# Kernel optimization log

Hardware: AMD Instinct MI355X
Metric: run time of the kernel (lower is better)

The kernel has to match this reference:

```python
import jax, jax.numpy as jnp
import numpy as np

B, S, D, H = 8, 4096, 1024, 16
DH = D // H  # head size = 64


def setup_inputs() -> dict:
    key = jax.random.key(0)
    ks = jax.random.split(key, 9)
    scale = 1.0 / np.sqrt(D)
    x = jax.random.normal(ks[0], (B, S, D), dtype=jnp.float32)
    wq = jax.random.normal(ks[1], (D, D), dtype=jnp.float32) * scale
    bq = jnp.zeros((D,), dtype=jnp.float32)
    wk = jax.random.normal(ks[2], (D, D), dtype=jnp.float32) * scale
    bk = jnp.zeros((D,), dtype=jnp.float32)
    wv = jax.random.normal(ks[3], (D, D), dtype=jnp.float32) * scale
    bv = jnp.zeros((D,), dtype=jnp.float32)
    wo = jax.random.normal(ks[4], (D, D), dtype=jnp.float32) * scale
    bo = jnp.zeros((D,), dtype=jnp.float32)
    return {"x": x, "wq": wq, "bq": bq, "wk": wk, "bk": bk,
            "wv": wv, "bv": bv, "wo": wo, "bo": bo}


def reference(x, wq, bq, wk, bk, wv, bv, wo, bo):
    b, s, d = x.shape
    # torch Linear: y = x @ W^T + b
    q = (x @ wq.T + bq).reshape(b, s, H, DH)
    k = (x @ wk.T + bk).reshape(b, s, H, DH)
    v = (x @ wv.T + bv).reshape(b, s, H, DH)
    # NOTE: original transpose_for_scores only reshapes (no permute), so
    # matmul(q, k.transpose(-1,-2)) contracts over head_size and the softmax
    # runs over the HEAD axis per token: scores shape [B, S, H, H].
    scores = jnp.einsum('bshd,bsgd->bshg', q, k) / jnp.sqrt(jnp.float32(DH))
    probs = jax.nn.softmax(scores, axis=-1)
    ctx = jnp.einsum('bshg,bsgd->bshd', probs, v).reshape(b, s, d)
    return ctx @ wo.T + bo
```

## Files before the change

### kernel.cpp

```cpp
#include <hip/hip_runtime.h>
#include <hip/hip_bf16.h>


#define DEV static __device__ __forceinline__

typedef __attribute__((ext_vector_type(8))) _Float16 fp16x8;
typedef __attribute__((ext_vector_type(4))) float f32x4;

DEV unsigned short f2h(float f) {
    union { _Float16 h; unsigned short u; } c;
    c.h = (_Float16)f;
    return c.u;
}
DEV float h2f(unsigned short u) {
    union { _Float16 h; unsigned short u; } c;
    c.u = u;
    return (float)c.h;
}

DEV void gl_lds16(const void* g, void* l) {
    __builtin_amdgcn_global_load_lds(
        (const __attribute__((address_space(1))) unsigned int*)g,
        (__attribute__((address_space(3))) unsigned int*)l, 16, 0, 0);
}

__global__ __launch_bounds__(256) void k_convert(
    const float* __restrict__ x,
    const float* __restrict__ wq, const float* __restrict__ wk,
    const float* __restrict__ wv, const float* __restrict__ wo,
    const float* __restrict__ bq, const float* __restrict__ bk,
    const float* __restrict__ bv,
    unsigned short* __restrict__ Xb, unsigned short* __restrict__ Wb,
    unsigned short* __restrict__ Wob, float* __restrict__ biasc)
{
    const int NX = 33554432 / 4;
    const int NW = 3145728 / 4;
    const int NO = 1048576 / 4;
    const int NB = 3072 / 4;
    const int total = NX + NW + NO + NB;
    for (int c = blockIdx.x * blockDim.x + threadIdx.x; c < total;
         c += gridDim.x * blockDim.x) {
        if (c < NX) {
            float4 v = ((const float4*)x)[c];
            uint2 u;
            u.x = f2h(v.x) | ((unsigned int)f2h(v.y) << 16);
            u.y = f2h(v.z) | ((unsigned int)f2h(v.w) << 16);
            ((uint2*)Xb)[c] = u;
        } else if (c < NX + NW) {
            int e = c - NX;
            const float* w = (e < 262144) ? wq : (e < 524288) ? wk : wv;
            int off = e & 262143;
            float4 v = ((const float4*)w)[off];
            uint2 u;
            u.x = f2h(v.x) | ((unsigned int)f2h(v.y) << 16);
            u.y = f2h(v.z) | ((unsigned int)f2h(v.w) << 16);
            ((uint2*)Wb)[e] = u;
        } else if (c < NX + NW + NO) {
            int e = c - NX - NW;
            float4 v = ((const float4*)wo)[e];
            uint2 u;
            u.x = f2h(v.x) | ((unsigned int)f2h(v.y) << 16);
            u.y = f2h(v.z) | ((unsigned int)f2h(v.w) << 16);
            ((uint2*)Wob)[e] = u;
        } else {
            int e = c - NX - NW - NO;
            const float* b = (e < 256) ? bq : (e < 512) ? bk : bv;
            int off = e & 255;
            ((float4*)biasc)[e] = ((const float4*)b)[off];
        }
    }
}

template <int LDA, bool OUT_F16>
__global__ __launch_bounds__(256) void k_gemm_bt(
    const unsigned short* __restrict__ A,
    const unsigned short* __restrict__ B,
    const float* __restrict__ bias,
    unsigned short* __restrict__ Ch,
    float* __restrict__ Cf,
    int ldc)
{
    __shared__ __align__(16) unsigned short As[128 * 32];
    __shared__ __align__(16) unsigned short Bs[128 * 32];

    const int tid  = threadIdx.x;
    const int lane = tid & 63;
    const int w    = tid >> 6;
    const int wr   = w >> 1, wc = w & 1;
    const int quad = lane >> 4;
    const int lr   = lane & 15;

    const int m0 = blockIdx.y * 128;
    const int n0 = blockIdx.x * 128;

    f32x4 acc[4][4];
#pragma unroll
    for (int i = 0; i < 4; ++i)
#pragma unroll
        for (int j = 0; j < 4; ++j) {
            f32x4 z = {0.f, 0.f, 0.f, 0.f};
            acc[i][j] = z;
        }

    const int id0 = tid, id1 = tid + 256;
    const int ar0 = id0 >> 2, ac0 = (id0 & 3) * 8;
    const int ar1 = id1 >> 2, ac1 = (id1 & 3) * 8;
    const unsigned short* Arow0 = A + (size_t)(m0 + ar0) * LDA + ac0;
    const unsigned short* Arow1 = A + (size_t)(m0 + ar1) * LDA + ac1;
    const unsigned short* Brow0 = B + (size_t)(n0 + ar0) * 1024 + ac0;
    const unsigned short* Brow1 = B + (size_t)(n0 + ar1) * 1024 + ac1;

    for (int k0 = 0; k0 < 1024; k0 += 32) {
        __syncthreads();
        gl_lds16(Arow0 + k0, (char*)As + id0 * 16);
        gl_lds16(Arow1 + k0, (char*)As + id1 * 16);
        gl_lds16(Brow0 + k0, (char*)Bs + id0 * 16);
        gl_lds16(Brow1 + k0, (char*)Bs + id1 * 16);
        asm volatile("s_waitcnt vmcnt(0)" ::: "memory");
        __syncthreads();

        fp16x8 a[4], b[4];
#pragma unroll
        for (int i = 0; i < 4; ++i)
            a[i] = *(const fp16x8*)(const void*)&As[(wr * 64 + i * 16 + lr) * 32 + quad * 8];
#pragma unroll
        for (int j = 0; j < 4; ++j)
            b[j] = *(const fp16x8*)(const void*)&Bs[(wc * 64 + j * 16 + lr) * 32 + quad * 8];
#pragma unroll
        for (int i = 0; i < 4; ++i)
#pragma unroll
            for (int j = 0; j < 4; ++j)
                acc[i][j] = __builtin_amdgcn_mfma_f32_16x16x32_f16(a[i], b[j], acc[i][j], 0, 0, 0);
    }

    float bj[4];
#pragma unroll
    for (int j = 0; j < 4; ++j) bj[j] = bias[n0 + wc * 64 + j * 16 + lr];
#pragma unroll
    for (int i = 0; i < 4; ++i) {
        const int mrow = m0 + wr * 64 + i * 16 + quad * 4;
#pragma unroll
        for (int j = 0; j < 4; ++j) {
            const int ncol = n0 + wc * 64 + j * 16 + lr;
#pragma unroll
            for (int r = 0; r < 4; ++r) {
                float v = acc[i][j][r] + bj[j];
                if (OUT_F16)
                    Ch[(size_t)(mrow + r) * ldc + ncol] = f2h(v);
                else
                    Cf[(size_t)(mrow + r) * ldc + ncol] = v;
            }
        }
    }
}

__global__ __launch_bounds__(256) void k_attn(unsigned short* __restrict__ qkv)
{
    __shared__ __align__(16) float sq[4][3072];
    __shared__ __align__(16) float sp[4][16 * 17];

    const int tid = threadIdx.x;
    const int wv  = tid >> 6;
    const int l   = tid & 63;
    const int t   = blockIdx.x * 4 + wv;
    unsigned short* tok = qkv + (size_t)t * 3072;

#pragma unroll
    for (int i = 0; i < 6; ++i) {
        const int e = i * 512 + l * 8;
        uint4 u = *(const uint4*)(tok + e);
        unsigned int uu[4] = {u.x, u.y, u.z, u.w};
#pragma unroll
        for (int c = 0; c < 4; ++c) {
            sq[wv][e + 2 * c]     = h2f((unsigned short)(uu[c] & 0xffff));
            sq[wv][e + 2 * c + 1] = h2f((unsigned short)(uu[c] >> 16));
        }
    }
    __syncthreads();

    const int h  = l >> 2;
    const int gq = (l & 3) * 4;
    const float4* q4 = (const float4*)&sq[wv][h * 64];
    const float4* k4 = (const float4*)&sq[wv][1024];

    float s[4] = {0.f, 0.f, 0.f, 0.f};
#pragma unroll
    for (int d4 = 0; d4 < 16; ++d4) {
        float4 qv = q4[d4];
#pragma unroll
        for (int g = 0; g < 4; ++g) {
            float4 kv = k4[(gq + g) * 16 + d4];
            s[g] += qv.x * kv.x + qv.y * kv.y + qv.z * kv.z + qv.w * kv.w;
        }
    }
#pragma unroll
    for (int g = 0; g < 4; ++g) s[g] *= 0.125f;

    float m = fmaxf(fmaxf(s[0], s[1]), fmaxf(s[2], s[3]));
    m = fmaxf(m, __shfl_xor(m, 1, 64));
    m = fmaxf(m, __shfl_xor(m, 2, 64));
    float e4[4], sum = 0.f;
#pragma unroll
    for (int g = 0; g < 4; ++g) { e4[g] = __expf(s[g] - m); sum += e4[g]; }
    sum += __shfl_xor(sum, 1, 64);
    sum += __shfl_xor(sum, 2, 64);
    const float inv = 1.0f / sum;
#pragma unroll
    for (int g = 0; g < 4; ++g) sp[wv][h * 17 + gq + g] = e4[g] * inv;
    __syncthreads();

    const int db = l & 3;
    const float4* v4 = (const float4*)&sq[wv][2048];
    float acc[16];
#pragma unroll
    for (int j = 0; j < 16; ++j) acc[j] = 0.f;
#pragma unroll
    for (int g = 0; g < 16; ++g) {
        const float p = sp[wv][h * 17 + g];
        const float4* vr = v4 + g * 16 + db * 4;
#pragma unroll
        for (int c = 0; c < 4; ++c) {
            float4 vvv = vr[c];
            acc[c * 4 + 0] += p * vvv.x;
            acc[c * 4 + 1] += p * vvv.y;
            acc[c * 4 + 2] += p * vvv.z;
            acc[c * 4 + 3] += p * vvv.w;
        }
    }

    unsigned short* dst = tok + h * 64 + db * 16;
    unsigned int o[8];
#pragma unroll
    for (int j = 0; j < 8; ++j)
        o[j] = f2h(acc[2 * j]) | ((unsigned int)f2h(acc[2 * j + 1]) << 16);
    uint4 o0 = {o[0], o[1], o[2], o[3]};
    uint4 o1 = {o[4], o[5], o[6], o[7]};
    ((uint4*)dst)[0] = o0;
    ((uint4*)dst)[1] = o1;
}

extern "C" void kernel_launch(void* const* d_in, const int* in_sizes, int n_in,
                              void* d_out, int out_size, void* d_ws, size_t ws_size,
                              hipStream_t stream)
{
    (void)in_sizes; (void)n_in; (void)out_size;

    const float* x  = (const float*)d_in[0];
    const float* wq = (const float*)d_in[1];
    const float* bq = (const float*)d_in[2];
    const float* wk = (const float*)d_in[3];
    const float* bk = (const float*)d_in[4];
    const float* wv = (const float*)d_in[5];
    const float* bv = (const float*)d_in[6];
    const float* wo = (const float*)d_in[7];
    const float* bo = (const float*)d_in[8];

    if (ws_size < 276836352ull) return;

    char* ws = (char*)d_ws;
    unsigned short* QKV  = (unsigned short*)(ws);
    unsigned short* Xb   = (unsigned short*)(ws + 201326592);
    unsigned short* Wb   = (unsigned short*)(ws + 268435456);
    unsigned short* Wob  = (unsigned short*)(ws + 274726912);
    float*          bqkv = (float*)(ws + 276824064);

    k_convert<<<2048, 256, 0, stream>>>(x, wq, wk, wv, wo, bq, bk, bv,
                                        Xb, Wb, Wob, bqkv);
    k_gemm_bt<1024, true><<<dim3(24, 256), 256, 0, stream>>>(
        Xb, Wb, bqkv, QKV, nullptr, 3072);
    k_attn<<<8192, 256, 0, stream>>>(QKV);
    k_gemm_bt<3072, false><<<dim3(8, 256), 256, 0, stream>>>(
        QKV, Wob, bo, nullptr, (float*)d_out, 1024);
}
```

Baseline: 696.7 us.

## Compute per-token head attention with fp16 MFMA instead of scalar fp32 LDS math

Rewrites the per-token head-axis attention kernel to stage Q and K as fp16 in padded LDS rows and compute the 16x16 score matrix with a 16x16x32 f16 MFMA. It then does the softmax with cross-lane shuffles and forms P·V with MFMA, reading V straight from global memory. This drops the fp32 conversion into LDS, cuts LDS footprint, and replaces scalar FMA loops, aiming to speed up a small part of a pipeline dominated by GEMMs. Risks include fp16 rounding of the probabilities, half-empty MFMA inputs padded with zeros, uncoalesced scalar V loads, and barriers swapped for plain waitcnt, which relies on intra-wave LDS ordering.

```diff
diff --git a/kernel.cpp b/kernel.cpp
--- a/kernel.cpp
+++ b/kernel.cpp
@@ -12,10 +12,10 @@
     c.h = (_Float16)f;
     return c.u;
 }
-DEV float h2f(unsigned short u) {
+DEV _Float16 u2h(unsigned short u) {
     union { _Float16 h; unsigned short u; } c;
     c.u = u;
-    return (float)c.h;
+    return c.h;
 }
 
 DEV void gl_lds16(const void* g, void* l) {
@@ -156,87 +156,89 @@
 
 __global__ __launch_bounds__(256) void k_attn(unsigned short* __restrict__ qkv)
 {
-    __shared__ __align__(16) float sq[4][3072];
-    __shared__ __align__(16) float sp[4][16 * 17];
-
-    const int tid = threadIdx.x;
-    const int wv  = tid >> 6;
-    const int l   = tid & 63;
-    const int t   = blockIdx.x * 4 + wv;
+    __shared__ __align__(16) unsigned short sqk[4][32 * 72];
+    __shared__ __align__(16) unsigned short sp[4][16 * 24];
+
+    const int tid  = threadIdx.x;
+    const int wv   = tid >> 6;
+    const int l    = tid & 63;
+    const int t    = blockIdx.x * 4 + wv;
     unsigned short* tok = qkv + (size_t)t * 3072;
 
-#pragma unroll
-    for (int i = 0; i < 6; ++i) {
-        const int e = i * 512 + l * 8;
-        uint4 u = *(const uint4*)(tok + e);
-        unsigned int uu[4] = {u.x, u.y, u.z, u.w};
-#pragma unroll
-        for (int c = 0; c < 4; ++c) {
-            sq[wv][e + 2 * c]     = h2f((unsigned short)(uu[c] & 0xffff));
-            sq[wv][e + 2 * c + 1] = h2f((unsigned short)(uu[c] >> 16));
-        }
-    }
-    __syncthreads();
-
-    const int h  = l >> 2;
-    const int gq = (l & 3) * 4;
-    const float4* q4 = (const float4*)&sq[wv][h * 64];
-    const float4* k4 = (const float4*)&sq[wv][1024];
-
-    float s[4] = {0.f, 0.f, 0.f, 0.f};
-#pragma unroll
-    for (int d4 = 0; d4 < 16; ++d4) {
-        float4 qv = q4[d4];
-#pragma unroll
-        for (int g = 0; g < 4; ++g) {
-            float4 kv = k4[(gq + g) * 16 + d4];
-            s[g] += qv.x * kv.x + qv.y * kv.y + qv.z * kv.z + qv.w * kv.w;
-        }
-    }
-#pragma unroll
-    for (int g = 0; g < 4; ++g) s[g] *= 0.125f;
-
-    float m = fmaxf(fmaxf(s[0], s[1]), fmaxf(s[2], s[3]));
-    m = fmaxf(m, __shfl_xor(m, 1, 64));
-    m = fmaxf(m, __shfl_xor(m, 2, 64));
-    float e4[4], sum = 0.f;
-#pragma unroll
-    for (int g = 0; g < 4; ++g) { e4[g] = __expf(s[g] - m); sum += e4[g]; }
-    sum += __shfl_xor(sum, 1, 64);
-    sum += __shfl_xor(sum, 2, 64);
-    const float inv = 1.0f / sum;
-#pragma unroll
-    for (int g = 0; g < 4; ++g) sp[wv][h * 17 + gq + g] = e4[g] * inv;
-    __syncthreads();
-
-    const int db = l & 3;
-    const float4* v4 = (const float4*)&sq[wv][2048];
-    float acc[16];
-#pragma unroll
-    for (int j = 0; j < 16; ++j) acc[j] = 0.f;
-#pragma unroll
-    for (int g = 0; g < 16; ++g) {
-        const float p = sp[wv][h * 17 + g];
-        const float4* vr = v4 + g * 16 + db * 4;
-#pragma unroll
-        for (int c = 0; c < 4; ++c) {
-            float4 vvv = vr[c];
-            acc[c * 4 + 0] += p * vvv.x;
-            acc[c * 4 + 1] += p * vvv.y;
-            acc[c * 4 + 2] += p * vvv.z;
-            acc[c * 4 + 3] += p * vvv.w;
-        }
-    }
-
-    unsigned short* dst = tok + h * 64 + db * 16;
-    unsigned int o[8];
-#pragma unroll
-    for (int j = 0; j < 8; ++j)
-        o[j] = f2h(acc[2 * j]) | ((unsigned int)f2h(acc[2 * j + 1]) << 16);
-    uint4 o0 = {o[0], o[1], o[2], o[3]};
-    uint4 o1 = {o[4], o[5], o[6], o[7]};
-    ((uint4*)dst)[0] = o0;
-    ((uint4*)dst)[1] = o1;
+    unsigned short* qk = sqk[wv];
+    unsigned short* pp = sp[wv];
+
+    const int quad = l >> 4;
+    const int lr   = l & 15;
+
+    {
+        const int d  = (l & 7) * 8;
+        const int r0 = l >> 3;
+#pragma unroll
+        for (int i = 0; i < 4; ++i) {
+            const int row = i * 8 + r0;
+            uint4 u = *(const uint4*)(tok + i * 512 + l * 8);
+            *(uint4*)&qk[row * 72 + d] = u;
+        }
+    }
+    asm volatile("s_waitcnt lgkmcnt(0)" ::: "memory");
+
+    f32x4 s = {0.f, 0.f, 0.f, 0.f};
+#pragma unroll
+    for (int ks = 0; ks < 2; ++ks) {
+        fp16x8 aq = *(const fp16x8*)(const void*)&qk[lr * 72 + ks * 32 + quad * 8];
+        fp16x8 bk = *(const fp16x8*)(const void*)&qk[(16 + lr) * 72 + ks * 32 + quad * 8];
+        s = __builtin_amdgcn_mfma_f32_16x16x32_f16(aq, bk, s, 0, 0, 0);
+    }
+
+#pragma unroll
+    for (int r = 0; r < 4; ++r) {
+        float sv = s[r] * 0.125f;
+        float m = sv;
+        m = fmaxf(m, __shfl_xor(m, 1, 64));
+        m = fmaxf(m, __shfl_xor(m, 2, 64));
+        m = fmaxf(m, __shfl_xor(m, 4, 64));
+        m = fmaxf(m, __shfl_xor(m, 8, 64));
+        float e = __expf(sv - m);
+        float su = e;
+        su += __shfl_xor(su, 1, 64);
+        su += __shfl_xor(su, 2, 64);
+        su += __shfl_xor(su, 4, 64);
+        su += __shfl_xor(su, 8, 64);
+        float p = e * __builtin_amdgcn_rcpf(su);
+        pp[(quad * 4 + r) * 24 + lr] = f2h(p);
+    }
+    asm volatile("s_waitcnt lgkmcnt(0)" ::: "memory");
+
+    fp16x8 pa;
+    if (quad < 2) {
+        pa = *(const fp16x8*)(const void*)&pp[lr * 24 + quad * 8];
+    } else {
+#pragma unroll
+        for (int j = 0; j < 8; ++j) pa[j] = (_Float16)0.f;
+    }
+
+    const unsigned short* vbase = tok + 2048;
+    f32x4 c[4];
+#pragma unroll
+    for (int nb = 0; nb < 4; ++nb) {
+        fp16x8 bv;
+#pragma unroll
+        for (int j = 0; j < 8; ++j) bv[j] = (_Float16)0.f;
+        if (quad < 2) {
+#pragma unroll
+            for (int j = 0; j < 8; ++j)
+                bv[j] = u2h(vbase[(quad * 8 + j) * 64 + nb * 16 + lr]);
+        }
+        f32x4 z = {0.f, 0.f, 0.f, 0.f};
+        c[nb] = __builtin_amdgcn_mfma_f32_16x16x32_f16(pa, bv, z, 0, 0, 0);
+    }
+
+#pragma unroll
+    for (int nb = 0; nb < 4; ++nb)
+#pragma unroll
+        for (int r = 0; r < 4; ++r)
+            tok[(quad * 4 + r) * 64 + nb * 16 + lr] = f2h(c[nb][r]);
 }
 
 extern "C" void kernel_launch(void* const* d_in, const int* in_sizes, int n_in,
```

Measured after the change: 643.2 us. 1.08x faster.
